# Performance work log

Hardware: AMD Instinct MI355X
Metric: run time of the kernel (lower is better)

Reference implementation:

```python
import jax, jax.numpy as jnp
import numpy as np


def _scan_dir(x, Wih, Whh, b, reverse):
    # x: (B,T,D); Wih: (4H,D); Whh: (4H,H); b: (4H,)  (= b_ih+b_hh)
    B = x.shape[0]
    H = Whh.shape[1]
    xg = jnp.einsum('btd,gd->btg', x, Wih) + b          # (B,T,4H) precomputed input projections
    xg = jnp.swapaxes(xg, 0, 1)                          # (T,B,4H)

    def step(carry, g_t):
        h, c = carry
        g = g_t + h @ Whh.T
        i, f, gg, o = jnp.split(g, 4, axis=-1)           # PyTorch gate order: i,f,g,o
        c = jax.nn.sigmoid(f) * c + jax.nn.sigmoid(i) * jnp.tanh(gg)
        h = jax.nn.sigmoid(o) * jnp.tanh(c)
        return (h, c), h

    h0 = jnp.zeros((B, H), x.dtype)
    _, hs = jax.lax.scan(step, (h0, h0), xg, reverse=reverse)
    return jnp.swapaxes(hs, 0, 1)                        # (B,T,H), time order preserved


def _bilstm(x, Wih_f, Whh_f, b_f, Wih_b, Whh_b, b_b):
    out_f = _scan_dir(x, Wih_f, Whh_f, b_f, reverse=False)
    out_b = _scan_dir(x, Wih_b, Whh_b, b_b, reverse=True)
    return jnp.concatenate([out_f, out_b], axis=-1)      # (B,T,2H)


def setup_inputs() -> dict:
    key = jax.random.key(0)
    ks = iter(jax.random.split(key, 32))
    B, T = 1024, 128
    H1, H2 = 50, 150

    def p(shape, scale):
        return (jax.random.normal(next(ks), shape, dtype=jnp.float32) * scale)

    s1 = 1.0 / np.sqrt(H1)
    s2 = 1.0 / np.sqrt(H2)
    inp = {
        'x': jax.random.normal(next(ks), (B, 1, T), dtype=jnp.float32),
        'rrs': jax.random.normal(next(ks), (B, 4), dtype=jnp.float32),
        # layer 1: in_dim=1, H=50, bidirectional
        'l1_Wih_f': p((4 * H1, 1), s1), 'l1_Whh_f': p((4 * H1, H1), s1), 'l1_b_f': p((4 * H1,), s1),
        'l1_Wih_b': p((4 * H1, 1), s1), 'l1_Whh_b': p((4 * H1, H1), s1), 'l1_b_b': p((4 * H1,), s1),
        # layer 2: in_dim=100, H=150, bidirectional
        'l2_Wih_f': p((4 * H2, 2 * H1), s2), 'l2_Whh_f': p((4 * H2, H2), s2), 'l2_b_f': p((4 * H2,), s2),
        'l2_Wih_b': p((4 * H2, 2 * H1), s2), 'l2_Whh_b': p((4 * H2, H2), s2), 'l2_b_b': p((4 * H2,), s2),
        # heads
        'head_W': p((20, 2 * H2), 0.05), 'head_b': p((20,), 0.05),
        'pef1_W': p((10, 4), 0.05), 'pef1_b': p((10,), 0.05),
        'pef2_W': p((2, 10), 0.05), 'pef2_b': p((2,), 0.05),
        'fc_W': p((4, 30), 0.05), 'fc_b': p((4,), 0.05),
    }
    return inp


def reference(x, rrs,
              l1_Wih_f, l1_Whh_f, l1_b_f, l1_Wih_b, l1_Whh_b, l1_b_b,
              l2_Wih_f, l2_Whh_f, l2_b_f, l2_Wih_b, l2_Whh_b, l2_b_b,
              head_W, head_b, pef1_W, pef1_b, pef2_W, pef2_b, fc_W, fc_b):
    xt = jnp.transpose(x, (0, 2, 1))                     # (B,T,1)
    out1 = _bilstm(xt, l1_Wih_f, l1_Whh_f, l1_b_f, l1_Wih_b, l1_Whh_b, l1_b_b)   # (B,T,100)
    out2 = _bilstm(out1, l2_Wih_f, l2_Whh_f, l2_b_f, l2_Wih_b, l2_Whh_b, l2_b_b) # (B,T,300)
    net = out2[:, -1]                                    # (B,300)
    waveform_feat = jax.nn.leaky_relu(net @ head_W.T + head_b, 0.3)              # (B,20)
    pef = jax.nn.leaky_relu(rrs @ pef1_W.T + pef1_b, 0.3)                        # (B,10)
    pef_logits = pef @ pef2_W.T + pef2_b                                         # (B,2)
    feat = jnp.concatenate([waveform_feat, pef], axis=1)                         # (B,30)
    logits = feat @ fc_W.T + fc_b                                                # (B,4)
    return (waveform_feat, pef_logits, feat, logits)
```

## Files before the change

### kernel.cpp

```cpp
#include <hip/hip_runtime.h>


typedef unsigned short u16;
typedef unsigned int u32;
typedef float f32x4 __attribute__((ext_vector_type(4)));
typedef _Float16 f16x8 __attribute__((ext_vector_type(8)));
typedef short s16x8 __attribute__((ext_vector_type(8)));

#if __has_builtin(__builtin_amdgcn_mfma_f32_16x16x32_f16)
#define USE_F16 1
#else
#define USE_F16 0
#endif

#define B1 1024
#define TT 128

__device__ __forceinline__ u16 to_h(float x) {
#if USE_F16
    _Float16 h = (_Float16)x;
    return __builtin_bit_cast(u16, h);
#else
    u32 u = __builtin_bit_cast(u32, x);
    u32 r = u + 0x7FFFu + ((u >> 16) & 1u);
    return (u16)(r >> 16);
#endif
}
__device__ __forceinline__ float from_h(u16 s) {
#if USE_F16
    return (float)__builtin_bit_cast(_Float16, s);
#else
    u32 u = ((u32)s) << 16;
    return __builtin_bit_cast(float, u);
#endif
}

__device__ __forceinline__ f32x4 mfma16(uint4 a, uint4 b, f32x4 c) {
#if USE_F16
    return __builtin_amdgcn_mfma_f32_16x16x32_f16(
        __builtin_bit_cast(f16x8, a), __builtin_bit_cast(f16x8, b), c, 0, 0, 0);
#else
    return __builtin_amdgcn_mfma_f32_16x16x32_bf16(
        __builtin_bit_cast(s16x8, a), __builtin_bit_cast(s16x8, b), c, 0, 0, 0);
#endif
}

#define LOG2E 1.4426950408889634f
__device__ __forceinline__ float sigm(float x) {
    return __builtin_amdgcn_rcpf(1.f + __builtin_amdgcn_exp2f(-LOG2E * x));
}
__device__ __forceinline__ float tanh_(float x) {
    return 1.f - 2.f * __builtin_amdgcn_rcpf(1.f + __builtin_amdgcn_exp2f(2.f * LOG2E * x));
}
__device__ __forceinline__ float clampf(float x, float k) {
    return fminf(fmaxf(x, -k), k);
}

__device__ __forceinline__ float lstm_cell(float ig, float fg, float gg, float og,
                                           float& c)
{
    float ei = __builtin_amdgcn_exp2f(-LOG2E * ig);
    float ef = __builtin_amdgcn_exp2f(-LOG2E * fg);
    float eg = __builtin_amdgcn_exp2f(2.f * LOG2E * clampf(gg, 15.f));
    float P   = (1.f + ei) * (eg + 1.f);
    float num = fmaf(c, P, (eg - 1.f) * (1.f + ef));
    float cn  = num * __builtin_amdgcn_rcpf((1.f + ef) * P);
    c = cn;
    float eo = __builtin_amdgcn_exp2f(-LOG2E * og);
    float ec = __builtin_amdgcn_exp2f(2.f * LOG2E * clampf(cn, 15.f));
    return (ec - 1.f) * __builtin_amdgcn_rcpf((1.f + eo) * (ec + 1.f));
}

__device__ __forceinline__ void wg_barrier_lds() {
    __builtin_amdgcn_sched_barrier(0);
    asm volatile("s_waitcnt lgkmcnt(0)" ::: "memory");
    __builtin_amdgcn_s_barrier();
    __builtin_amdgcn_sched_barrier(0);
}

__device__ __forceinline__ void prep_frag_body(
    const float* __restrict__ Wih, const float* __restrict__ Whh,
    const float* __restrict__ bias, uint4* __restrict__ dst,
    int GR, int KT, int x_off, int x_len, int h_off, int h_len, int bias_k,
    int bid, int l)
{
    int tile = bid / KT, kt = bid - tile * KT;
    int ml = l & 15;
    int qq = ml >> 2, tau = ml & 3;
    int jj = tile * 4 + qq;
    bool valid = jj < GR;
    int row = tau * GR + jj;
    u32 dw[4];
    #pragma unroll
    for (int d = 0; d < 4; ++d) {
        u16 hh[2];
        #pragma unroll
        for (int s = 0; s < 2; ++s) {
            int j = d * 2 + s;
            int k = kt * 32 + (l >> 4) * 8 + j;
            float val = 0.f;
            if (valid) {
                if (k >= x_off && k < x_off + x_len) val = Wih[row * x_len + (k - x_off)];
                else if (k >= h_off && k < h_off + h_len) val = Whh[row * h_len + (k - h_off)];
                else if (k == bias_k) val = bias[row];
            }
            hh[s] = to_h(val);
        }
        dw[d] = (u32)hh[0] | ((u32)hh[1] << 16);
    }
    uint4 o; o.x = dw[0]; o.y = dw[1]; o.z = dw[2]; o.w = dw[3];
    dst[bid * 64 + l] = o;
}

__global__ void prep_all(const float* __restrict__ W1ihF, const float* __restrict__ W1hhF,
                         const float* __restrict__ b1F,
                         const float* __restrict__ W1ihB, const float* __restrict__ W1hhB,
                         const float* __restrict__ b1B,
                         const float* __restrict__ W2ihF, const float* __restrict__ W2hhF,
                         const float* __restrict__ b2F, const float* __restrict__ W2ihB,
                         uint4* __restrict__ frag1f, uint4* __restrict__ frag1b,
                         uint4* __restrict__ frag2f, float* __restrict__ WtT)
{
    int bid = blockIdx.x;
    int l = threadIdx.x;
    if (bid < 32)
        prep_frag_body(W1ihF, W1hhF, b1F, frag1f, 50, 2, 0, 1, 1, 50, 63, bid, l);
    else if (bid < 64)
        prep_frag_body(W1ihB, W1hhB, b1B, frag1b, 50, 2, 0, 1, 1, 50, 63, bid - 32, l);
    else if (bid < 384)
        prep_frag_body(W2ihF, W2hhF, b2F, frag2f, 150, 8, 0, 100, 100, 150, 255, bid - 64, l);
    else {
        int idx = (bid - 384) * 64 + l;
        if (idx < 60000) {
            int k = idx / 600, g = idx - k * 600;
            WtT[idx] = W2ihB[g * 100 + k];
        }
    }
}

__global__ __launch_bounds__(512, 2) void l1_scan(
    const float* __restrict__ x, const uint4* __restrict__ fragF,
    const uint4* __restrict__ fragB, u16* __restrict__ out1f)
{
    const int tid = threadIdx.x;
    const int lane = tid & 63;
    const int w = tid >> 6;
    const int q = lane >> 4;
    const int b = lane & 15;
    const int blk = blockIdx.x;
    const int dir = blockIdx.y;
    const uint4* frag = dir ? fragB : fragF;

    __shared__ u16 v[2][1024];
    __shared__ float x_s[128][17];

    uint4 af[2][2];
    #pragma unroll
    for (int p = 0; p < 2; ++p)
        #pragma unroll
        for (int kt = 0; kt < 2; ++kt)
            af[p][kt] = frag[((w + 8 * p) * 2 + kt) * 64 + lane];

    const int b0 = blk * 16;
    for (int idx = tid; idx < 1024; idx += 512) ((u32*)v)[idx] = 0u;
    for (int idx = tid; idx < 2048; idx += 512) {
        int bb = idx >> 7, t = idx & 127;
        x_s[t][bb] = x[(size_t)(b0 + bb) * TT + t];
    }
    __syncthreads();
    const u16 oneh = to_h(1.0f);
    if (tid < 16) {
        v[0][(112 + tid) * 8 + 7] = oneh;
        v[1][(112 + tid) * 8 + 7] = oneh;
        v[0][tid * 8] = to_h(x[(size_t)(b0 + tid) * TT + (dir ? TT - 1 : 0)]);
    }
    int vslot[2]; size_t eb[2];
    #pragma unroll
    for (int p = 0; p < 2; ++p) {
        int jj = (w + 8 * p) * 4 + q;
        int k1 = 1 + (jj < 50 ? jj : 0);
        vslot[p] = ((k1 >> 5) * 64 + ((k1 & 31) >> 3) * 16 + b) * 8 + (k1 & 7);
        int k2 = dir * 50 + (jj < 50 ? jj : 0);
        eb[p] = (((size_t)blk * 4 + (k2 >> 5)) * 64
                 + ((k2 & 31) >> 3) * 16 + b) * 8 + (k2 & 7);
    }
    float c[2] = {0.f, 0.f};
    __syncthreads();

#define L1_STEP(T, CUR) { \
    uint4 bf0 = *(const uint4*)&v[CUR][lane * 8]; \
    uint4 bf1 = *(const uint4*)&v[CUR][(64 + lane) * 8]; \
    f32x4 acc[2]; \
    _Pragma("unroll") for (int p = 0; p < 2; ++p) { \
        acc[p] = mfma16(af[p][0], bf0, (f32x4){0.f, 0.f, 0.f, 0.f}); \
        acc[p] = mfma16(af[p][1], bf1, acc[p]); \
    } \
    const int tt = dir ? 127 - (T) : (T); \
    _Pragma("unroll") for (int p = 0; p < 2; ++p) { \
        int jj = (w + 8 * p) * 4 + q; \
        if (jj < 50) { \
            float hn = lstm_cell(acc[p][0], acc[p][1], acc[p][2], acc[p][3], c[p]); \
            u16 hb = to_h(hn); \
            out1f[eb[p] + (size_t)tt * 131072] = hb; \
            v[1 - (CUR)][vslot[p]] = hb; \
        } \
    } \
    if (tid < 16 && (T) < 127) \
        v[1 - (CUR)][tid * 8] = to_h(x_s[dir ? 126 - (T) : (T) + 1][tid]); \
    wg_barrier_lds(); }

    for (int t2 = 0; t2 < TT; t2 += 2) {
        L1_STEP(t2, 0)
        L1_STEP(t2 + 1, 1)
    }
#undef L1_STEP
}

__global__ __launch_bounds__(512, 2) void l2f_scan(
    const uint4* __restrict__ frag, const u16* __restrict__ out1f,
    float* __restrict__ net)
{
    const int tid = threadIdx.x;
    const int lane = tid & 63;
    const int w = tid >> 6;
    const int q = lane >> 4;
    const int b = lane & 15;
    const int blk = blockIdx.x;
    const int b0 = blk * 16;
    const uint4* o4 = (const uint4*)out1f;

    __shared__ u16 v[2][4096];

    uint4 af[5][8];
    #pragma unroll
    for (int i = 0; i < 5; ++i)
        #pragma unroll
        for (int kt = 0; kt < 8; ++kt)
            af[i][kt] = frag[((w + 8 * i) * 8 + kt) * 64 + lane];

    for (int idx = tid; idx < 4096; idx += 512) ((u32*)v)[idx] = 0u;

    uint4 pfA[4], pfB[4];
    #pragma unroll
    for (int ktx = 0; ktx < 4; ++ktx) {
        pfA[ktx] = o4[((size_t)(0 * 64 + blk) * 4 + ktx) * 64 + lane];
        pfB[ktx] = o4[((size_t)(1 * 64 + blk) * 4 + ktx) * 64 + lane];
    }

    __syncthreads();
    const u16 oneh = to_h(1.0f);
    if (tid < 16) {
        v[0][(496 + tid) * 8 + 7] = oneh;
        v[1][(496 + tid) * 8 + 7] = oneh;
    }
    if (w == 0 && lane < 16) {
        uint2 xv; xv.x = pfA[3].x; xv.y = pfA[3].y;
        *(uint2*)&v[0][(192 + lane) * 8] = xv;
    }

    int vslot[5];
    #pragma unroll
    for (int p = 0; p < 5; ++p) {
        int jj = (w + 8 * p) * 4 + q;
        int k = 100 + (jj < 150 ? jj : 0);
        vslot[p] = ((k >> 5) * 64 + ((k & 31) >> 3) * 16 + b) * 8 + (k & 7);
    }
    float c[5] = {0.f, 0.f, 0.f, 0.f, 0.f};
    __syncthreads();

#define L2F_STEP(T, CUR, PFC, PFD) { \
    uint4 bfu[5]; \
    _Pragma("unroll") for (int kh = 0; kh < 5; ++kh) \
        bfu[kh] = *(const uint4*)&v[CUR][((kh + 3) * 64 + lane) * 8]; \
    f32x4 acc[5]; \
    _Pragma("unroll") for (int p = 0; p < 5; ++p) { \
        acc[p] = mfma16(af[p][0], PFC[0], (f32x4){0.f, 0.f, 0.f, 0.f}); \
        acc[p] = mfma16(af[p][1], PFC[1], acc[p]); \
        acc[p] = mfma16(af[p][2], PFC[2], acc[p]); \
    } \
    const int tn = ((T) < 126) ? (T) + 2 : 127; \
    _Pragma("unroll") for (int ktx = 0; ktx < 4; ++ktx) \
        PFC[ktx] = o4[(((size_t)tn * 64 + blk) * 4 + ktx) * 64 + lane]; \
    _Pragma("unroll") for (int kh = 0; kh < 4; ++kh) { \
        _Pragma("unroll") for (int p = 0; p < 5; ++p) \
            acc[p] = mfma16(af[p][kh + 3], bfu[kh], acc[p]); \
    } \
    _Pragma("unroll") for (int p = 0; p < 5; ++p) { \
        acc[p] = mfma16(af[p][7], bfu[4], acc[p]); \
        int jj = (w + 8 * p) * 4 + q; \
        if (jj < 150) { \
            float hn = lstm_cell(acc[p][0], acc[p][1], acc[p][2], acc[p][3], c[p]); \
            v[1 - (CUR)][vslot[p]] = to_h(hn); \
            if ((T) == 127) net[(size_t)(b0 + b) * 300 + jj] = hn; \
        } \
    } \
    if (w == 0 && lane < 16) { \
        uint2 xv; xv.x = PFD[3].x; xv.y = PFD[3].y; \
        *(uint2*)&v[1 - (CUR)][(192 + lane) * 8] = xv; \
    } \
    wg_barrier_lds(); }

    for (int t2 = 0; t2 < TT; t2 += 2) {
        L2F_STEP(t2, 0, pfA, pfB)
        L2F_STEP(t2 + 1, 1, pfB, pfA)
    }
#undef L2F_STEP
}

__global__ __launch_bounds__(640, 1) void l2b_step(
    const u16* __restrict__ out1f, const float* __restrict__ WtT,
    const float* __restrict__ bias, float* __restrict__ net)
{
    const int tid = threadIdx.x;
    const int blk = blockIdx.x;
    const int b0 = blk * 16;
    __shared__ alignas(16) float x_s[100][16];
    __shared__ alignas(16) float gbuf[16][644];
    for (int idx = tid; idx < 1600; idx += 640) {
        int k2 = idx >> 4, bb = idx & 15;
        x_s[k2][bb] = from_h(out1f[((((size_t)127 * 64 + blk) * 4 + (k2 >> 5)) * 64
                                    + ((k2 & 31) >> 3) * 16 + bb) * 8 + (k2 & 7)]);
    }
    __syncthreads();
    if (tid < 600) {
        int g = tid;
        float acc[16];
        #pragma unroll
        for (int bb = 0; bb < 16; ++bb) acc[bb] = 0.f;
        for (int k = 0; k < 100; ++k) {
            float wv = WtT[k * 600 + g];
            float4 xa = *(const float4*)&x_s[k][0];
            float4 xb = *(const float4*)&x_s[k][4];
            float4 xc = *(const float4*)&x_s[k][8];
            float4 xd = *(const float4*)&x_s[k][12];
            acc[0] = fmaf(wv, xa.x, acc[0]);  acc[1] = fmaf(wv, xa.y, acc[1]);
            acc[2] = fmaf(wv, xa.z, acc[2]);  acc[3] = fmaf(wv, xa.w, acc[3]);
            acc[4] = fmaf(wv, xb.x, acc[4]);  acc[5] = fmaf(wv, xb.y, acc[5]);
            acc[6] = fmaf(wv, xb.z, acc[6]);  acc[7] = fmaf(wv, xb.w, acc[7]);
            acc[8] = fmaf(wv, xc.x, acc[8]);  acc[9] = fmaf(wv, xc.y, acc[9]);
            acc[10] = fmaf(wv, xc.z, acc[10]); acc[11] = fmaf(wv, xc.w, acc[11]);
            acc[12] = fmaf(wv, xd.x, acc[12]); acc[13] = fmaf(wv, xd.y, acc[13]);
            acc[14] = fmaf(wv, xd.z, acc[14]); acc[15] = fmaf(wv, xd.w, acc[15]);
        }
        #pragma unroll
        for (int bb = 0; bb < 16; ++bb) gbuf[bb][g] = acc[bb];
    }
    __syncthreads();
    for (int idx = tid; idx < 2400; idx += 640) {
        int j = idx >> 4, bb = idx & 15;
        float ig = gbuf[bb][j]       + bias[j];
        float gg = gbuf[bb][j + 300] + bias[j + 300];
        float og = gbuf[bb][j + 450] + bias[j + 450];
        float cn = sigm(ig) * tanh_(gg);
        float hn = sigm(og) * tanh_(cn);
        net[(size_t)(b0 + bb) * 300 + 150 + j] = hn;
    }
}

__global__ void head1(const float* __restrict__ net, const float* __restrict__ rrs,
                      const float* __restrict__ headW, const float* __restrict__ headb,
                      const float* __restrict__ p1W, const float* __restrict__ p1b,
                      const float* __restrict__ p2W, const float* __restrict__ p2b,
                      float* __restrict__ out)
{
    int gid = blockIdx.x * 256 + threadIdx.x;
    int b = gid >> 2, og = gid & 3;
    float acc[5];
    #pragma unroll
    for (int o2 = 0; o2 < 5; ++o2) acc[o2] = headb[og * 5 + o2];
    const float* nb = net + (size_t)b * 300;
    for (int k = 0; k < 300; ++k) {
        float nv = nb[k];
        #pragma unroll
        for (int o2 = 0; o2 < 5; ++o2)
            acc[o2] = fmaf(headW[(og * 5 + o2) * 300 + k], nv, acc[o2]);
    }
    #pragma unroll
    for (int o2 = 0; o2 < 5; ++o2) {
        int o = og * 5 + o2;
        float vv = acc[o2] > 0.f ? acc[o2] : 0.3f * acc[o2];
        out[b * 20 + o] = vv;
        out[22528 + b * 30 + o] = vv;
    }
    if (og == 0) {
        float p[10];
        #pragma unroll
        for (int r = 0; r < 10; ++r) {
            float a = p1b[r];
            #pragma unroll
            for (int qq = 0; qq < 4; ++qq) a = fmaf(p1W[r * 4 + qq], rrs[b * 4 + qq], a);
            p[r] = a > 0.f ? a : 0.3f * a;
            out[22528 + b * 30 + 20 + r] = p[r];
        }
        #pragma unroll
        for (int s = 0; s < 2; ++s) {
            float a = p2b[s];
            #pragma unroll
            for (int r = 0; r < 10; ++r) a = fmaf(p2W[s * 10 + r], p[r], a);
            out[20480 + b * 2 + s] = a;
        }
    }
}

__global__ void head2(const float* __restrict__ fcW, const float* __restrict__ fcb,
                      float* __restrict__ out)
{
    int b = blockIdx.x * 256 + threadIdx.x;
    const float* feat = out + 22528 + b * 30;
    float f[30];
    #pragma unroll
    for (int k = 0; k < 30; ++k) f[k] = feat[k];
    #pragma unroll
    for (int s = 0; s < 4; ++s) {
        float a = fcb[s];
        #pragma unroll
        for (int k = 0; k < 30; ++k) a = fmaf(fcW[s * 30 + k], f[k], a);
        out[53248 + b * 4 + s] = a;
    }
}

extern "C" void kernel_launch(void* const* d_in, const int* in_sizes, int n_in,
                              void* d_out, int out_size, void* d_ws, size_t ws_size,
                              hipStream_t stream)
{
    const float* x     = (const float*)d_in[0];
    const float* rrs   = (const float*)d_in[1];
    const float* W1ihF = (const float*)d_in[2];
    const float* W1hhF = (const float*)d_in[3];
    const float* b1F   = (const float*)d_in[4];
    const float* W1ihB = (const float*)d_in[5];
    const float* W1hhB = (const float*)d_in[6];
    const float* b1B   = (const float*)d_in[7];
    const float* W2ihF = (const float*)d_in[8];
    const float* W2hhF = (const float*)d_in[9];
    const float* b2F   = (const float*)d_in[10];
    const float* W2ihB = (const float*)d_in[11];
    const float* b2B   = (const float*)d_in[13];
    const float* headW = (const float*)d_in[14];
    const float* headb = (const float*)d_in[15];
    const float* p1W   = (const float*)d_in[16];
    const float* p1b   = (const float*)d_in[17];
    const float* p2W   = (const float*)d_in[18];
    const float* p2b   = (const float*)d_in[19];
    const float* fcW   = (const float*)d_in[20];
    const float* fcb   = (const float*)d_in[21];
    float* out = (float*)d_out;

    char* ws = (char*)d_ws;
    uint4* frag1f = (uint4*)(ws + 0);
    uint4* frag1b = (uint4*)(ws + 32768);
    uint4* frag2f = (uint4*)(ws + 65536);
    float* WtT    = (float*)(ws + 393216);
    u16*   out1f  = (u16*)(ws + 655360);
    float* net    = (float*)(ws + 655360 + 33554432);
    (void)ws_size; (void)in_sizes; (void)n_in; (void)out_size;

    prep_all<<<1322, 64, 0, stream>>>(W1ihF, W1hhF, b1F, W1ihB, W1hhB, b1B,
                                      W2ihF, W2hhF, b2F, W2ihB,
                                      frag1f, frag1b, frag2f, WtT);
    l1_scan<<<dim3(64, 2), 512, 0, stream>>>(x, frag1f, frag1b, out1f);
    l2f_scan<<<64, 512, 0, stream>>>(frag2f, out1f, net);
    l2b_step<<<64, 640, 0, stream>>>(out1f, WtT, b2B, net);
    head1<<<16, 256, 0, stream>>>(net, rrs, headW, headb, p1W, p1b, p2W, p2b, out);
    head2<<<4, 256, 0, stream>>>(fcW, fcb, out);
}
```

Before: 280.8 us.

## Pipeline next-step input MFMAs with the LSTM cell and fold log2e into weights

The layer-2 forward recurrence now issues the next timestep's input-projection MFMAs, which do not depend on h, inside the current step's cell-update loop. This uses double-buffered accumulators, so the matrix and transcendental work can overlap across the serial dependency. The LOG2E and 2*LOG2E gate scaling is folded into the fp16 weight fragments during prep, which removes per-element multiplies in the cell. The prefetch pointer now advances without clamping, so the last steps read past the end of the buffer, though that data is never used. Folding the scale into fp16 weights also slightly changes rounding.

```diff
diff --git a/kernel.cpp b/kernel.cpp
--- a/kernel.cpp
+++ b/kernel.cpp
@@ -56,17 +56,17 @@
     return fminf(fmaxf(x, -k), k);
 }
 
-__device__ __forceinline__ float lstm_cell(float ig, float fg, float gg, float og,
-                                           float& c)
-{
-    float ei = __builtin_amdgcn_exp2f(-LOG2E * ig);
-    float ef = __builtin_amdgcn_exp2f(-LOG2E * fg);
-    float eg = __builtin_amdgcn_exp2f(2.f * LOG2E * clampf(gg, 15.f));
+__device__ __forceinline__ float lstm_cell(float ig2, float fg2, float gg2,
+                                           float og2, float& c)
+{
+    float ei = __builtin_amdgcn_exp2f(-ig2);
+    float ef = __builtin_amdgcn_exp2f(-fg2);
+    float eg = __builtin_amdgcn_exp2f(clampf(gg2, 43.28f));
     float P   = (1.f + ei) * (eg + 1.f);
     float num = fmaf(c, P, (eg - 1.f) * (1.f + ef));
     float cn  = num * __builtin_amdgcn_rcpf((1.f + ef) * P);
     c = cn;
-    float eo = __builtin_amdgcn_exp2f(-LOG2E * og);
+    float eo = __builtin_amdgcn_exp2f(-og2);
     float ec = __builtin_amdgcn_exp2f(2.f * LOG2E * clampf(cn, 15.f));
     return (ec - 1.f) * __builtin_amdgcn_rcpf((1.f + eo) * (ec + 1.f));
 }
@@ -90,6 +90,7 @@
     int jj = tile * 4 + qq;
     bool valid = jj < GR;
     int row = tau * GR + jj;
+    float rowscale = (tau == 2) ? 2.0f * LOG2E : LOG2E;
     u32 dw[4];
     #pragma unroll
     for (int d = 0; d < 4; ++d) {
@@ -104,7 +105,7 @@
                 else if (k >= h_off && k < h_off + h_len) val = Whh[row * h_len + (k - h_off)];
                 else if (k == bias_k) val = bias[row];
             }
-            hh[s] = to_h(val);
+            hh[s] = to_h(val * rowscale);
         }
         dw[d] = (u32)hh[0] | ((u32)hh[1] << 16);
     }
@@ -240,12 +241,14 @@
 
     for (int idx = tid; idx < 4096; idx += 512) ((u32*)v)[idx] = 0u;
 
+    const uint4* pfp = o4 + (size_t)blk * 256 + lane;
     uint4 pfA[4], pfB[4];
     #pragma unroll
-    for (int ktx = 0; ktx < 4; ++ktx) {
-        pfA[ktx] = o4[((size_t)(0 * 64 + blk) * 4 + ktx) * 64 + lane];
-        pfB[ktx] = o4[((size_t)(1 * 64 + blk) * 4 + ktx) * 64 + lane];
-    }
+    for (int ktx = 0; ktx < 4; ++ktx) pfA[ktx] = pfp[ktx * 64];
+    pfp += 16384;
+    #pragma unroll
+    for (int ktx = 0; ktx < 4; ++ktx) pfB[ktx] = pfp[ktx * 64];
+    pfp += 16384;
 
     __syncthreads();
     const u16 oneh = to_h(1.0f);
@@ -266,43 +269,47 @@
         vslot[p] = ((k >> 5) * 64 + ((k & 31) >> 3) * 16 + b) * 8 + (k & 7);
     }
     float c[5] = {0.f, 0.f, 0.f, 0.f, 0.f};
-    __syncthreads();
-
-#define L2F_STEP(T, CUR, PFC, PFD) { \
+
+    f32x4 accA[5], accB[5];
+    #pragma unroll
+    for (int p = 0; p < 5; ++p) {
+        accA[p] = mfma16(af[p][0], pfA[0], (f32x4){0.f, 0.f, 0.f, 0.f});
+        accA[p] = mfma16(af[p][1], pfA[1], accA[p]);
+        accA[p] = mfma16(af[p][2], pfA[2], accA[p]);
+    }
+    __syncthreads();
+
+#define L2F_STEP(T, CUR, ACCC, ACCN, PFREF, PFOTH) { \
     uint4 bfu[5]; \
     _Pragma("unroll") for (int kh = 0; kh < 5; ++kh) \
         bfu[kh] = *(const uint4*)&v[CUR][((kh + 3) * 64 + lane) * 8]; \
-    f32x4 acc[5]; \
+    _Pragma("unroll") for (int kh = 0; kh < 5; ++kh) { \
+        _Pragma("unroll") for (int p = 0; p < 5; ++p) \
+            ACCC[p] = mfma16(af[p][kh + 3], bfu[kh], ACCC[p]); \
+    } \
+    _Pragma("unroll") for (int ktx = 0; ktx < 4; ++ktx) \
+        PFREF[ktx] = pfp[ktx * 64]; \
+    pfp += 16384; \
     _Pragma("unroll") for (int p = 0; p < 5; ++p) { \
-        acc[p] = mfma16(af[p][0], PFC[0], (f32x4){0.f, 0.f, 0.f, 0.f}); \
-        acc[p] = mfma16(af[p][1], PFC[1], acc[p]); \
-        acc[p] = mfma16(af[p][2], PFC[2], acc[p]); \
-    } \
-    const int tn = ((T) < 126) ? (T) + 2 : 127; \
-    _Pragma("unroll") for (int ktx = 0; ktx < 4; ++ktx) \
-        PFC[ktx] = o4[(((size_t)tn * 64 + blk) * 4 + ktx) * 64 + lane]; \
-    _Pragma("unroll") for (int kh = 0; kh < 4; ++kh) { \
-        _Pragma("unroll") for (int p = 0; p < 5; ++p) \
-            acc[p] = mfma16(af[p][kh + 3], bfu[kh], acc[p]); \
-    } \
-    _Pragma("unroll") for (int p = 0; p < 5; ++p) { \
-        acc[p] = mfma16(af[p][7], bfu[4], acc[p]); \
+        ACCN[p] = mfma16(af[p][0], PFOTH[0], (f32x4){0.f, 0.f, 0.f, 0.f}); \
+        ACCN[p] = mfma16(af[p][1], PFOTH[1], ACCN[p]); \
+        ACCN[p] = mfma16(af[p][2], PFOTH[2], ACCN[p]); \
         int jj = (w + 8 * p) * 4 + q; \
         if (jj < 150) { \
-            float hn = lstm_cell(acc[p][0], acc[p][1], acc[p][2], acc[p][3], c[p]); \
+            float hn = lstm_cell(ACCC[p][0], ACCC[p][1], ACCC[p][2], ACCC[p][3], c[p]); \
             v[1 - (CUR)][vslot[p]] = to_h(hn); \
             if ((T) == 127) net[(size_t)(b0 + b) * 300 + jj] = hn; \
         } \
     } \
     if (w == 0 && lane < 16) { \
-        uint2 xv; xv.x = PFD[3].x; xv.y = PFD[3].y; \
+        uint2 xv; xv.x = PFOTH[3].x; xv.y = PFOTH[3].y; \
         *(uint2*)&v[1 - (CUR)][(192 + lane) * 8] = xv; \
     } \
     wg_barrier_lds(); }
 
     for (int t2 = 0; t2 < TT; t2 += 2) {
-        L2F_STEP(t2, 0, pfA, pfB)
-        L2F_STEP(t2 + 1, 1, pfB, pfA)
+        L2F_STEP(t2, 0, accA, accB, pfA, pfB)
+        L2F_STEP(t2 + 1, 1, accB, accA, pfB, pfA)
     }
 #undef L2F_STEP
 }
```

Result: faster. 274.5 us (-2.2%).
